# Kernel tuning notes

Hardware: AMD Instinct MI355X
Metric: run time of the kernel (lower is better)

The kernel has to match this reference:

```python
import jax, jax.numpy as jnp
import numpy as np

B, C, H, W = 16, 3, 224, 224
P = 16
DIM = 256
NL = 8
DS = 16          # d_state (mamba default)
DCONV = 4
NCLS = 1000
DI = 2 * DIM     # expand * dim
DTR = -(-DIM // 16)  # dt_rank = ceil(dim/16)
NPATCH = (H // P) * (W // P)
SEQ = NPATCH + 1


def _ln(x, g, b, eps=1e-5):
    mu = x.mean(-1, keepdims=True)
    var = ((x - mu) ** 2).mean(-1, keepdims=True)
    return (x - mu) * jax.lax.rsqrt(var + eps) * g + b


def setup_inputs() -> dict:
    key = jax.random.key(0)
    ks = jax.random.split(key, 12)
    pd = C * P * P
    s = 0.02
    return dict(
        img=jax.random.normal(ks[0], (B, C, H, W), jnp.float32),
        pe_ln1_g=jnp.ones((pd,), jnp.float32), pe_ln1_b=jnp.zeros((pd,), jnp.float32),
        pe_w=jax.random.normal(ks[1], (pd, DIM), jnp.float32) * s,
        pe_b=jnp.zeros((DIM,), jnp.float32),
        pe_ln2_g=jnp.ones((DIM,), jnp.float32), pe_ln2_b=jnp.zeros((DIM,), jnp.float32),
        pos_emb=jax.random.normal(ks[2], (1, SEQ, DIM), jnp.float32) * s,
        cls_tok=jax.random.normal(ks[3], (1, 1, DIM), jnp.float32) * s,
        ln_w=jnp.ones((NL, DIM), jnp.float32), ln_b=jnp.zeros((NL, DIM), jnp.float32),
        in_w=jax.random.normal(ks[4], (NL, DIM, 2 * DI), jnp.float32) * s,
        conv_w=jax.random.normal(ks[5], (NL, DI, DCONV), jnp.float32) * s,
        conv_b=jnp.zeros((NL, DI), jnp.float32),
        xproj_w=jax.random.normal(ks[6], (NL, DI, DTR + 2 * DS), jnp.float32) * s,
        dtproj_w=jax.random.normal(ks[7], (NL, DTR, DI), jnp.float32) * s,
        dtproj_b=jax.random.uniform(ks[8], (NL, DI), jnp.float32, -4.0, -2.0),
        A_log=jnp.log(jnp.broadcast_to(jnp.arange(1, DS + 1, dtype=jnp.float32), (NL, DI, DS))) + jnp.zeros((NL, DI, DS), jnp.float32),
        Dp=jnp.ones((NL, DI), jnp.float32),
        out_w=jax.random.normal(ks[9], (NL, DI, DIM), jnp.float32) * s,
        normf_w=jnp.ones((DIM,), jnp.float32), normf_b=jnp.zeros((DIM,), jnp.float32),
        head_w=jax.random.normal(ks[10], (DIM, NCLS), jnp.float32) * s,
        head_b=jnp.zeros((NCLS,), jnp.float32),
    )


def _mamba(x, in_w, conv_w, conv_b, xproj_w, dtproj_w, dtproj_b, A_log, Dp, out_w):
    b, L, _ = x.shape
    xz = x @ in_w                       # (b, L, 2*DI)
    xm, z = jnp.split(xz, 2, axis=-1)
    # causal depthwise conv1d (torch pads both sides then slices -> left-pad d_conv-1)
    xc = jnp.pad(xm.transpose(0, 2, 1), ((0, 0), (0, 0), (DCONV - 1, 0)))
    xc = jax.lax.conv_general_dilated(
        xc, conv_w[:, None, :], (1,), 'VALID',
        dimension_numbers=('NCH', 'OIH', 'NCH'), feature_group_count=DI)
    u = jax.nn.silu(xc + conv_b[None, :, None]).transpose(0, 2, 1)  # (b, L, DI)
    dbc = u @ xproj_w                   # (b, L, DTR+2*DS)
    dt, Bm, Cm = jnp.split(dbc, [DTR, DTR + DS], axis=-1)
    dt = jax.nn.softplus(dt @ dtproj_w + dtproj_b)  # (b, L, DI)
    A = -jnp.exp(A_log)                 # (DI, DS)

    def step(h, inp):
        dt_t, B_t, C_t, u_t = inp       # (b,DI), (b,DS), (b,DS), (b,DI)
        dA = jnp.exp(dt_t[:, :, None] * A)                 # (b, DI, DS)
        h = dA * h + (dt_t * u_t)[:, :, None] * B_t[:, None, :]
        y = jnp.einsum('bdn,bn->bd', h, C_t)
        return h, y

    h0 = jnp.zeros((b, DI, DS), x.dtype)
    xs = (dt.transpose(1, 0, 2), Bm.transpose(1, 0, 2),
          Cm.transpose(1, 0, 2), u.transpose(1, 0, 2))
    _, ys = jax.lax.scan(step, h0, xs)
    y = ys.transpose(1, 0, 2) + u * Dp  # (b, L, DI)
    y = y * jax.nn.silu(z)
    return y @ out_w                    # (b, L, DIM)


def reference(img, pe_ln1_g, pe_ln1_b, pe_w, pe_b, pe_ln2_g, pe_ln2_b, pos_emb,
              cls_tok, ln_w, ln_b, in_w, conv_w, conv_b, xproj_w, dtproj_w,
              dtproj_b, A_log, Dp, out_w, normf_w, normf_b, head_w, head_b):
    b = img.shape[0]
    h, w = H // P, W // P
    # 'b c (h p1) (w p2) -> b (h w) (p1 p2 c)'
    x = img.reshape(b, C, h, P, w, P).transpose(0, 2, 4, 3, 5, 1).reshape(b, h * w, P * P * C)
    x = _ln(x, pe_ln1_g, pe_ln1_b)
    x = x @ pe_w + pe_b
    x = _ln(x, pe_ln2_g, pe_ln2_b)
    x = jnp.concatenate([jnp.broadcast_to(cls_tok, (b, 1, DIM)), x], axis=1)
    x = x + pos_emb[:, :x.shape[1]]
    residual = None
    for i in range(NL):
        residual = x if residual is None else x + residual
        xn = _ln(residual, ln_w[i], ln_b[i])
        x = _mamba(xn, in_w[i], conv_w[i], conv_b[i], xproj_w[i],
                   dtproj_w[i], dtproj_b[i], A_log[i], Dp[i], out_w[i])
    residual = x + residual
    x = _ln(residual, normf_w, normf_b)
    x = x[:, 0]                          # pool == 'cls'
    return x @ head_w + head_b
```

## Files before the change

kernel.cpp:

```cpp
#include <hip/hip_runtime.h>
#include <math.h>

#define NB   16
#define SEQL 197
#define TB   (NB*SEQL)
#define DIMM 256
#define DI   512
#define DS   16
#define NL   8

typedef __bf16 bf16x8 __attribute__((ext_vector_type(8)));
typedef __bf16 bf16x4 __attribute__((ext_vector_type(4)));
typedef float floatx4 __attribute__((ext_vector_type(4)));

__device__ __forceinline__ void block_reduce_2(float& s1, float& s2, float* red, int tid){
  #pragma unroll
  for (int off = 32; off > 0; off >>= 1){
    s1 += __shfl_down(s1, off, 64);
    s2 += __shfl_down(s2, off, 64);
  }
  __syncthreads();
  if ((tid & 63) == 0){ red[(tid>>6)*2] = s1; red[(tid>>6)*2+1] = s2; }
  __syncthreads();
  s1 = red[0] + red[2] + red[4] + red[6];
  s2 = red[1] + red[3] + red[5] + red[7];
}

__global__ __launch_bounds__(256) void prep_weights(
    const float* __restrict__ in_w, const float* __restrict__ out_w,
    const float* __restrict__ pe_w, const float* __restrict__ xproj,
    __bf16* __restrict__ wt_in, __bf16* __restrict__ wt_out,
    __bf16* __restrict__ wt_pe, float* __restrict__ wt_xp_f)
{
  __shared__ float t[32][33];
  int bid = blockIdx.x;
  const float* src; __bf16* dst = nullptr; float* dstf = nullptr;
  int K, Nin, n0, k0;
  if (bid < 2048){
    int z = bid >> 8, tt = bid & 255;
    K = 256; Nin = 1024; n0 = (tt & 31)*32; k0 = (tt >> 5)*32;
    src = in_w  + (size_t)z*K*Nin;
    dst = wt_in + (size_t)z*K*Nin;
  } else if (bid < 3072){
    int t2 = bid - 2048; int z = t2 >> 7, tt = t2 & 127;
    K = 512; Nin = 256; n0 = (tt & 7)*32; k0 = (tt >> 3)*32;
    src = out_w  + (size_t)z*K*Nin;
    dst = wt_out + (size_t)z*K*Nin;
  } else if (bid < 3264){
    int tt = bid - 3072;
    K = 768; Nin = 256; n0 = (tt & 7)*32; k0 = (tt >> 3)*32;
    src = pe_w; dst = wt_pe;
  } else {
    int t2 = bid - 3264; int z = t2 >> 5, tt = t2 & 31;
    K = 512; Nin = 48; n0 = (tt & 1)*32; k0 = (tt >> 1)*32;
    src  = xproj + (size_t)z*K*Nin;
    dstf = wt_xp_f + (size_t)z*64*512;
  }
  int tx = threadIdx.x & 31, ty = threadIdx.x >> 5;
  #pragma unroll
  for (int j = 0; j < 4; j++){
    int n = n0 + tx;
    t[ty + j*8][tx] = (n < Nin) ? src[(size_t)(k0 + ty + j*8)*Nin + n] : 0.f;
  }
  __syncthreads();
  if (dstf){
    #pragma unroll
    for (int j = 0; j < 4; j++){
      int k = k0 + tx, c = n0 + ty + j*8;
      dstf[(size_t)(k>>2)*256 + c*4 + (k&3)] = t[tx][ty + j*8];
    }
  } else {
    #pragma unroll
    for (int j = 0; j < 4; j++)
      dst[(size_t)(n0 + ty + j*8)*K + k0 + tx] = (__bf16)t[tx][ty + j*8];
  }
}

template<int BM, int BN, int KS>
__global__ __launch_bounds__(256) void gemm_bf16(
    const __bf16* __restrict__ A, const __bf16* __restrict__ Wt,
    const float* __restrict__ bias, float* __restrict__ C, int M, int N, int K)
{
  constexpr int BK  = 32;
  constexpr int LDA = BK + 8;
  constexpr int TMW = BM/32;
  constexpr int TNW = BN/32;
  __shared__ __bf16 As[BM][LDA];
  __shared__ __bf16 Bs[BN][LDA];

  int tid  = threadIdx.x;
  int lane = tid & 63, w = tid >> 6;
  int wm = w >> 1, wn = w & 1;
  int l15 = lane & 15, quad = lane >> 4;
  int nt = blockIdx.x / KS, ks = blockIdx.x % KS;
  int bm = blockIdx.y * BM, bn = nt * BN;
  int kbeg = ks * (K / KS), kend = kbeg + (K / KS);

  floatx4 acc[TMW][TNW] = {};

  for (int k0 = kbeg; k0 < kend; k0 += BK){
    #pragma unroll
    for (int i = 0; i < BM/64; i++){
      int c = tid + i*256;
      int row = c >> 2, kc = c & 3;
      int m = bm + row;
      uint4 v = make_uint4(0,0,0,0);
      if (m < M) v = ((const uint4*)(A + (size_t)m*K + k0))[kc];
      *(uint4*)&As[row][kc*8] = v;
    }
    #pragma unroll
    for (int i = 0; i < BN/64; i++){
      int c = tid + i*256;
      int row = c >> 2, kc = c & 3;
      int n = bn + row;
      uint4 v = ((const uint4*)(Wt + (size_t)n*K + k0))[kc];
      *(uint4*)&Bs[row][kc*8] = v;
    }
    __syncthreads();
    bf16x8 af[TMW], bf[TNW];
    #pragma unroll
    for (int mi = 0; mi < TMW; mi++)
      af[mi] = *(const bf16x8*)&As[wm*(BM/2) + mi*16 + l15][quad*8];
    #pragma unroll
    for (int ni = 0; ni < TNW; ni++)
      bf[ni] = *(const bf16x8*)&Bs[wn*(BN/2) + ni*16 + l15][quad*8];
    #pragma unroll
    for (int mi = 0; mi < TMW; mi++)
      #pragma unroll
      for (int ni = 0; ni < TNW; ni++)
        acc[mi][ni] = __builtin_amdgcn_mfma_f32_16x16x32_bf16(af[mi], bf[ni], acc[mi][ni], 0, 0, 0);
    __syncthreads();
  }
  #pragma unroll
  for (int mi = 0; mi < TMW; mi++){
    #pragma unroll
    for (int ni = 0; ni < TNW; ni++){
      int col = bn + wn*(BN/2) + ni*16 + l15;
      float bv = (KS == 1 && bias) ? bias[col] : 0.f;
      #pragma unroll
      for (int r = 0; r < 4; r++){
        int row = bm + wm*(BM/2) + mi*16 + quad*4 + r;
        if (row < M){
          if (KS == 1) C[(size_t)row*N + col] = acc[mi][ni][r] + bv;
          else         atomicAdd(&C[(size_t)row*N + col], acc[mi][ni][r]);
        }
      }
    }
  }
}

template<int DO_LN>
__global__ __launch_bounds__(512) void gemm_out_fused(
    const __bf16* __restrict__ A, const __bf16* __restrict__ Wt,
    float* __restrict__ resid, __bf16* __restrict__ xn_bf,
    const float* __restrict__ g, const float* __restrict__ bta)
{
  constexpr int BK = 64, LDA = BK + 8;
  __shared__ alignas(16) char smem[(16 + 256) * LDA * sizeof(__bf16)];
  __bf16 (*As)[LDA] = (__bf16(*)[LDA])smem;
  __bf16 (*Bs)[LDA] = (__bf16(*)[LDA])(smem + 16*LDA*sizeof(__bf16));
  float  (*sy)[264] = (float(*)[264])smem;

  int tid = threadIdx.x, lane = tid & 63, w = tid >> 6;
  int l15 = lane & 15, quad = lane >> 4;
  int bm = blockIdx.x * 16;

  floatx4 acc[2] = {};
  for (int k0 = 0; k0 < 512; k0 += BK){
    if (tid < 128){
      int row = tid >> 3, kc = tid & 7;
      *(uint4*)&As[row][kc*8] = ((const uint4*)(A + (size_t)(bm+row)*512 + k0))[kc];
    }
    #pragma unroll
    for (int i = 0; i < 4; i++){
      int c = tid + i*512;
      int row = c >> 3, kc = c & 7;
      *(uint4*)&Bs[row][kc*8] = ((const uint4*)(Wt + (size_t)row*512 + k0))[kc];
    }
    __syncthreads();
    #pragma unroll
    for (int kk = 0; kk < 2; kk++){
      bf16x8 af = *(const bf16x8*)&As[l15][kk*32 + quad*8];
      #pragma unroll
      for (int ni = 0; ni < 2; ni++){
        bf16x8 bfv = *(const bf16x8*)&Bs[w*32 + ni*16 + l15][kk*32 + quad*8];
        acc[ni] = __builtin_amdgcn_mfma_f32_16x16x32_bf16(af, bfv, acc[ni], 0, 0, 0);
      }
    }
    __syncthreads();
  }
  #pragma unroll
  for (int ni = 0; ni < 2; ni++){
    int col = w*32 + ni*16 + l15;
    #pragma unroll
    for (int r = 0; r < 4; r++)
      sy[quad*4 + r][col] = acc[ni][r];
  }
  __syncthreads();
  #pragma unroll
  for (int rr = 0; rr < 2; rr++){
    int row = w*2 + rr;
    size_t base = (size_t)(bm + row)*256 + lane*4;
    float4 y4 = *(const float4*)&sy[row][lane*4];
    float4 rv = *(const float4*)&resid[base];
    float4 v;
    v.x = y4.x + rv.x; v.y = y4.y + rv.y; v.z = y4.z + rv.z; v.w = y4.w + rv.w;
    *(float4*)&resid[base] = v;
    if (DO_LN){
      float s  = v.x + v.y + v.z + v.w;
      float s2 = v.x*v.x + v.y*v.y + v.z*v.z + v.w*v.w;
      #pragma unroll
      for (int off = 1; off < 64; off <<= 1){
        s  += __shfl_xor(s,  off, 64);
        s2 += __shfl_xor(s2, off, 64);
      }
      float mu  = s * (1.f/256.f);
      float var = s2 * (1.f/256.f) - mu*mu;
      float rrq = rsqrtf(var + 1e-5f);
      float4 gv = *(const float4*)&g[lane*4];
      float4 bv = *(const float4*)&bta[lane*4];
      bf16x4 o;
      o[0] = (__bf16)((v.x - mu)*rrq*gv.x + bv.x);
      o[1] = (__bf16)((v.y - mu)*rrq*gv.y + bv.y);
      o[2] = (__bf16)((v.z - mu)*rrq*gv.z + bv.z);
      o[3] = (__bf16)((v.w - mu)*rrq*gv.w + bv.w);
      *(bf16x4*)&xn_bf[base] = o;
    }
  }
}

__global__ __launch_bounds__(256) void patch_ln1(
    const float* __restrict__ img, const float* __restrict__ g1, const float* __restrict__ b1,
    __bf16* __restrict__ xp_bf)
{
  __shared__ float red[8];
  int blk = blockIdx.x;
  int b = blk / 196, p = blk % 196;
  int hh = p / 14, ww = p % 14;
  int tid = threadIdx.x;

  float v[3]; float s = 0.f, s2 = 0.f;
  #pragma unroll
  for (int i = 0; i < 3; i++){
    int e  = tid + i*256;
    int c  = e % 3;
    int p2 = (e/3) % 16;
    int p1 = e / 48;
    float val = img[((b*3 + c)*224 + hh*16 + p1)*224 + ww*16 + p2];
    v[i] = val; s += val; s2 += val*val;
  }
  block_reduce_2(s, s2, red, tid);
  float mu = s * (1.f/768.f);
  float var = s2 * (1.f/768.f) - mu*mu;
  float rr = rsqrtf(var + 1e-5f);
  #pragma unroll
  for (int i = 0; i < 3; i++){
    int e = tid + i*256;
    xp_bf[(size_t)blk*768 + e] = (__bf16)((v[i] - mu) * rr * g1[e] + b1[e]);
  }
}

__global__ __launch_bounds__(256) void ln2_cls_pos(
    const float* __restrict__ pemb, const float* __restrict__ g2, const float* __restrict__ b2,
    const float* __restrict__ pos, const float* __restrict__ cls,
    float* __restrict__ resid,
    const float* __restrict__ g0, const float* __restrict__ b0,
    __bf16* __restrict__ xn_bf)
{
  __shared__ float red[8];
  int blk = blockIdx.x;
  int b = blk / SEQL, l = blk % SEQL;
  int tid = threadIdx.x;
  float o;
  if (l == 0){
    o = cls[tid] + pos[tid];
  } else {
    int p = l - 1;
    float v = pemb[(size_t)(b*196 + p)*256 + tid];
    float s = v, s2 = v*v;
    block_reduce_2(s, s2, red, tid);
    float mu = s * (1.f/256.f);
    float var = s2 * (1.f/256.f) - mu*mu;
    float rr = rsqrtf(var + 1e-5f);
    o = (v - mu) * rr * g2[tid] + b2[tid] + pos[l*256 + tid];
  }
  size_t idx = (size_t)blk*256 + tid;
  resid[idx] = o;
  float s = o, s2 = o*o;
  block_reduce_2(s, s2, red, tid);
  float mu = s * (1.f/256.f);
  float var = s2 * (1.f/256.f) - mu*mu;
  float rr = rsqrtf(var + 1e-5f);
  xn_bf[idx] = (__bf16)((o - mu) * rr * g0[tid] + b0[tid]);
}

__global__ __launch_bounds__(256) void conv_xproj(
    const float* __restrict__ xz, const float* __restrict__ cw, const float* __restrict__ cb,
    const float* __restrict__ wxp,
    float* __restrict__ u, float* __restrict__ dbc)
{
  __shared__ float s_u[8][512];
  __shared__ float s_acc[4][8][64];
  int tid = threadIdx.x;
  int t0 = blockIdx.x * 8;

  int d = (tid & 127) * 4;
  float4 w0 = *(const float4*)&cw[(d+0)*4];
  float4 w1 = *(const float4*)&cw[(d+1)*4];
  float4 w2 = *(const float4*)&cw[(d+2)*4];
  float4 w3 = *(const float4*)&cw[(d+3)*4];
  float4 cbv = *(const float4*)&cb[d];
  const float4 z4 = make_float4(0.f,0.f,0.f,0.f);
  int tt0 = t0 + (tid >> 7)*4;
  float4 h1 = (tt0 >= 1) ? *(const float4*)&xz[(size_t)(tt0-1)*1024 + d] : z4;
  float4 h2 = (tt0 >= 2) ? *(const float4*)&xz[(size_t)(tt0-2)*1024 + d] : z4;
  float4 h3 = (tt0 >= 3) ? *(const float4*)&xz[(size_t)(tt0-3)*1024 + d] : z4;
  int l0 = tt0 % SEQL;
  #pragma unroll
  for (int j = 0; j < 4; j++){
    int t = tt0 + j;
    int l = l0 + j; if (l >= SEQL) l -= SEQL;
    float4 x0 = *(const float4*)&xz[(size_t)t*1024 + d];
    float4 x1 = (l>=1) ? h1 : z4;
    float4 x2 = (l>=2) ? h2 : z4;
    float4 x3 = (l>=3) ? h3 : z4;
    float4 r = cbv;
    r.x += x3.x*w0.x + x2.x*w0.y + x1.x*w0.z + x0.x*w0.w;
    r.y += x3.y*w1.x + x2.y*w1.y + x1.y*w1.z + x0.y*w1.w;
    r.z += x3.z*w2.x + x2.z*w2.y + x1.z*w2.z + x0.z*w2.w;
    r.w += x3.w*w3.x + x2.w*w3.y + x1.w*w3.z + x0.w*w3.w;
    r.x *= 1.f/(1.f + __expf(-r.x));
    r.y *= 1.f/(1.f + __expf(-r.y));
    r.z *= 1.f/(1.f + __expf(-r.z));
    r.w *= 1.f/(1.f + __expf(-r.w));
    *(float4*)&u[(size_t)t*512 + d] = r;
    *(float4*)&s_u[(tid>>7)*4 + j][d] = r;
    h3 = h2; h2 = h1; h1 = x0;
  }
  __syncthreads();

  int col = tid & 63, sl = tid >> 6;
  const float4* wp4 = (const float4*)wxp + (size_t)sl*32*64 + col;
  float a[8] = {};
  #pragma unroll 4
  for (int k4 = 0; k4 < 32; k4++){
    float4 wv = wp4[(size_t)k4*64];
    #pragma unroll
    for (int t = 0; t < 8; t++){
      float4 v = *(const float4*)&s_u[t][sl*128 + k4*4];
      a[t] += wv.x*v.x + wv.y*v.y + wv.z*v.z + wv.w*v.w;
    }
  }
  #pragma unroll
  for (int t = 0; t < 8; t++) s_acc[sl][t][col] = a[t];
  __syncthreads();
  #pragma unroll
  for (int j = 0; j < 2; j++){
    int p = tid + j*256;
    int tok = p >> 6, c2 = p & 63;
    if (c2 < 48){
      float v = s_acc[0][tok][c2] + s_acc[1][tok][c2]
              + s_acc[2][tok][c2] + s_acc[3][tok][c2];
      dbc[(size_t)(t0 + tok)*64 + c2] = v;
    }
  }
}

#define SCT 32
#define NCH ((SEQL + SCT - 1)/SCT)
#define NDL 8
__global__ __launch_bounds__(128) void scan_kernel(
    const float* __restrict__ u, const float* __restrict__ dbc,
    const float* __restrict__ xz, const float* __restrict__ A_log, const float* __restrict__ Dp,
    const float* __restrict__ dtw, const float* __restrict__ dtb,
    __bf16* __restrict__ yg_bf)
{
  __shared__ float s_D [16][36];
  __shared__ float s_B [16][36];
  __shared__ float s_C [16][36];
  __shared__ float s_u [NDL][36];
  __shared__ float s_z [NDL][36];
  __shared__ float s_dt[NDL][36];
  __shared__ float s_yp[SCT][NDL][20];
  __shared__ float s_dp[NDL];

  int tid = threadIdx.x;
  int n = tid & 15, dl = tid >> 4;
  int b = blockIdx.x >> 6, dg = blockIdx.x & 63;
  int d0 = dg * NDL;
  const size_t base = (size_t)b * SEQL;

  float A = -__expf(A_log[(d0+dl)*DS + n]);
  float h = 0.f;
  if (tid < NDL) s_dp[tid] = Dp[d0 + tid];
  int cch = tid & 7;
  float wc[16];
  #pragma unroll
  for (int k = 0; k < 16; k++) wc[k] = dtw[k*512 + d0 + cch];
  float dtbv = dtb[d0 + cch];

  float r_u[2], r_z[2], r_db[12];
  auto load_regs = [&](int c){
    #pragma unroll
    for (int i = 0; i < 2; i++){
      int v = tid + i*128;
      int tg = c*SCT + (v>>3); if (tg > SEQL-1) tg = SEQL-1;
      size_t t = base + tg;
      r_u[i] = u [t*512 + d0 + (v&7)];
      r_z[i] = xz[t*1024 + 512 + d0 + (v&7)];
    }
    #pragma unroll
    for (int s = 0; s < 3; s++)
      #pragma unroll
      for (int i = 0; i < 4; i++){
        int v = tid + i*128;
        int tg = c*SCT + (v>>4); if (tg > SEQL-1) tg = SEQL-1;
        r_db[s*4+i] = dbc[(base + tg)*64 + s*16 + (v&15)];
      }
  };
  auto write_DBC = [&](){
    #pragma unroll
    for (int i = 0; i < 4; i++){
      int v = tid + i*128;
      s_D[v&15][v>>4] = r_db[0+i];
      s_B[v&15][v>>4] = r_db[4+i];
      s_C[v&15][v>>4] = r_db[8+i];
    }
  };
  auto write_UZ = [&](){
    #pragma unroll
    for (int i = 0; i < 2; i++){
      int v = tid + i*128;
      s_u[v&7][v>>3] = r_u[i];
      s_z[v&7][v>>3] = r_z[i];
    }
  };
  auto compute_dt = [&](){
    #pragma unroll
    for (int i = 0; i < 2; i++){
      int tl = (tid >> 3) + i*16;
      float acc = dtbv;
      #pragma unroll
      for (int k = 0; k < 16; k++) acc += s_D[k][tl] * wc[k];
      s_dt[cch][tl] = (acc > 20.f) ? acc : log1pf(__expf(acc));
    }
  };

  load_regs(0);
  write_DBC();
  write_UZ();
  __syncthreads();
  compute_dt();
  __syncthreads();

  for (int c = 0; c < NCH; c++){
    if (c + 1 < NCH) load_regs(c+1);

    float4 dt4, u4, B4, C4;
    #pragma unroll
    for (int tl = 0; tl < SCT; tl++){
      if ((tl & 3) == 0){
        dt4 = *(const float4*)&s_dt[dl][tl];
        u4  = *(const float4*)&s_u [dl][tl];
        B4  = *(const float4*)&s_B [n][tl];
        C4  = *(const float4*)&s_C [n][tl];
      }
      float dtv = ((float*)&dt4)[tl&3];
      float uv  = ((float*)&u4 )[tl&3];
      float Bv  = ((float*)&B4 )[tl&3];
      float Cv  = ((float*)&C4 )[tl&3];
      h = __expf(dtv * A) * h + (dtv * uv) * Bv;
      s_yp[tl][dl][n] = h * Cv;
    }
    __syncthreads();

    if (c + 1 < NCH) write_DBC();

    #pragma unroll
    for (int j = 0; j < 2; j++){
      int p = tid + j*128;
      int tl = p >> 3, dr = p & 7;
      float4 a0 = *(const float4*)&s_yp[tl][dr][0];
      float4 a1 = *(const float4*)&s_yp[tl][dr][4];
      float4 a2 = *(const float4*)&s_yp[tl][dr][8];
      float4 a3 = *(const float4*)&s_yp[tl][dr][12];
      float yv = ((a0.x+a0.y)+(a0.z+a0.w)) + ((a1.x+a1.y)+(a1.z+a1.w))
               + ((a2.x+a2.y)+(a2.z+a2.w)) + ((a3.x+a3.y)+(a3.z+a3.w));
      int tg = c*SCT + tl;
      if (tg < SEQL){
        float uv = s_u[dr][tl];
        float zv = s_z[dr][tl];
        float sg = 1.f / (1.f + __expf(-zv));
        yg_bf[(base + tg)*512 + d0 + dr] = (__bf16)((yv + uv*s_dp[dr]) * zv * sg);
      }
    }
    __syncthreads();

    if (c + 1 < NCH){
      write_UZ();
      compute_dt();
      __syncthreads();
    }
  }
}

__global__ __launch_bounds__(256) void final_head(
    const float* __restrict__ resid,
    const float* __restrict__ g, const float* __restrict__ bta,
    const float* __restrict__ head_w, const float* __restrict__ head_b,
    float* __restrict__ out)
{
  __shared__ float xs[16][256];
  int tid = threadIdx.x, lane = tid & 63, w = tid >> 6;
  #pragma unroll
  for (int rb = 0; rb < 4; rb++){
    int b = w + rb*4;
    const float* rp = resid + (size_t)b*SEQL*256;
    float4 v = *(const float4*)&rp[lane*4];
    float s  = v.x + v.y + v.z + v.w;
    float s2 = v.x*v.x + v.y*v.y + v.z*v.z + v.w*v.w;
    #pragma unroll
    for (int off = 1; off < 64; off <<= 1){
      s  += __shfl_xor(s,  off, 64);
      s2 += __shfl_xor(s2, off, 64);
    }
    float mu  = s * (1.f/256.f);
    float var = s2 * (1.f/256.f) - mu*mu;
    float rr  = rsqrtf(var + 1e-5f);
    float4 gv = *(const float4*)&g[lane*4];
    float4 bv = *(const float4*)&bta[lane*4];
    xs[b][lane*4+0] = (v.x - mu)*rr*gv.x + bv.x;
    xs[b][lane*4+1] = (v.y - mu)*rr*gv.y + bv.y;
    xs[b][lane*4+2] = (v.z - mu)*rr*gv.z + bv.z;
    xs[b][lane*4+3] = (v.w - mu)*rr*gv.w + bv.w;
  }
  __syncthreads();
  int nl = tid & 31, bq = tid >> 5;
  int nn = blockIdx.x*32 + nl;
  if (nn >= 1000) return;
  float acc0 = 0.f, acc1 = 0.f;
  #pragma unroll 8
  for (int k = 0; k < 256; k++){
    float wv = head_w[k*1000 + nn];
    acc0 += xs[bq][k]   * wv;
    acc1 += xs[bq+8][k] * wv;
  }
  float hb = head_b[nn];
  out[(size_t)bq*1000 + nn]     = acc0 + hb;
  out[(size_t)(bq+8)*1000 + nn] = acc1 + hb;
}

extern "C" void kernel_launch(void* const* d_in, const int* in_sizes, int n_in,
                              void* d_out, int out_size, void* d_ws, size_t ws_size,
                              hipStream_t stream) {
  const float* img   = (const float*)d_in[0];
  const float* ln1g  = (const float*)d_in[1];
  const float* ln1b  = (const float*)d_in[2];
  const float* pe_w  = (const float*)d_in[3];
  const float* pe_b  = (const float*)d_in[4];
  const float* ln2g  = (const float*)d_in[5];
  const float* ln2b  = (const float*)d_in[6];
  const float* pos   = (const float*)d_in[7];
  const float* cls   = (const float*)d_in[8];
  const float* ln_w  = (const float*)d_in[9];
  const float* ln_b  = (const float*)d_in[10];
  const float* in_w  = (const float*)d_in[11];
  const float* conv_w= (const float*)d_in[12];
  const float* conv_b= (const float*)d_in[13];
  const float* xproj = (const float*)d_in[14];
  const float* dtw   = (const float*)d_in[15];
  const float* dtb   = (const float*)d_in[16];
  const float* A_log = (const float*)d_in[17];
  const float* Dp    = (const float*)d_in[18];
  const float* out_w = (const float*)d_in[19];
  const float* nfw   = (const float*)d_in[20];
  const float* nfb   = (const float*)d_in[21];
  const float* head_w= (const float*)d_in[22];
  const float* head_b= (const float*)d_in[23];
  float* out = (float*)d_out;

  float* ws = (float*)d_ws;
  float* resid = ws;  ws += (size_t)TB*DIMM;
  float* xz    = ws;  ws += (size_t)TB*2*DI;
  float* u     = ws;  ws += (size_t)TB*DI;
  float* dbc   = ws;  ws += (size_t)TB*64;
  float* wt_xp_f = ws; ws += (size_t)NL*64*512;
  __bf16* xn_bf = (__bf16*)ws;  ws += (size_t)TB*DIMM/2;
  __bf16* yg_bf = (__bf16*)ws;  ws += (size_t)TB*DI/2;
  __bf16* wt_in = (__bf16*)ws;  ws += (size_t)NL*1024*256/2;
  __bf16* wt_out= (__bf16*)ws;  ws += (size_t)NL*256*512/2;
  __bf16* wt_pe = (__bf16*)ws;  ws += (size_t)256*768/2;
  __bf16* xp_bf = (__bf16*)xz;
  float*  pemb  = u;

  prep_weights<<<3520, 256, 0, stream>>>(in_w, out_w, pe_w, xproj,
                                          wt_in, wt_out, wt_pe, wt_xp_f);

  patch_ln1<<<NB*196, 256, 0, stream>>>(img, ln1g, ln1b, xp_bf);
  gemm_bf16<64,64,1><<<dim3(256/64, 3136/64), 256, 0, stream>>>(
      xp_bf, wt_pe, pe_b, pemb, 3136, 256, 768);
  ln2_cls_pos<<<NB*SEQL, 256, 0, stream>>>(pemb, ln2g, ln2b, pos, cls,
                                           resid, ln_w, ln_b, xn_bf);

  for (int i = 0; i < NL; i++){
    gemm_bf16<64,128,1><<<dim3(1024/128, (TB+63)/64), 256, 0, stream>>>(
        xn_bf, wt_in + (size_t)i*1024*256, nullptr, xz, TB, 1024, 256);
    conv_xproj<<<TB/8, 256, 0, stream>>>(
        xz, conv_w + i*DI*4, conv_b + i*DI, wt_xp_f + (size_t)i*64*512, u, dbc);
    scan_kernel<<<NB*64, 128, 0, stream>>>(
        u, dbc, xz, A_log + i*DI*DS, Dp + i*DI, dtw + i*16*DI, dtb + i*DI, yg_bf);
    if (i < NL-1)
      gemm_out_fused<1><<<TB/16, 512, 0, stream>>>(
          yg_bf, wt_out + (size_t)i*256*512, resid, xn_bf,
          ln_w + (i+1)*DIMM, ln_b + (i+1)*DIMM);
    else
      gemm_out_fused<0><<<TB/16, 512, 0, stream>>>(
          yg_bf, wt_out + (size_t)i*256*512, resid, nullptr, nullptr, nullptr);
  }
  final_head<<<(1000+31)/32, 256, 0, stream>>>(resid, nfw, nfb, head_w, head_b, out);
}
```

Before: 640.7 us.

## Prefetch GEMM tiles through registers, coalesce patch LN, use one wave per row

The bf16 GEMM now loads the next K-tile from global memory into registers while MFMAs run on the current LDS tile. The K-tile grows to 64 with an inner 32-step loop, and the unused split-K atomic path is removed. patch_ln1 now reads each pixel's three channels from contiguous rows, so image loads coalesce, and writes the permuted index directly. ln2_cls_pos handles one token per wave with float4 loads and shuffle reductions instead of block-wide reductions. The register prefetch raises register pressure, and the GEMMs plus LN kernels are a small share of the total time next to the scan.

After: 683.4 us. 1.07x slower.

```diff
diff --git a/kernel.cpp b/kernel.cpp
--- a/kernel.cpp
+++ b/kernel.cpp
@@ -76,15 +76,17 @@
   }
 }
 
-template<int BM, int BN, int KS>
+template<int BM, int BN, int BK>
 __global__ __launch_bounds__(256) void gemm_bf16(
     const __bf16* __restrict__ A, const __bf16* __restrict__ Wt,
     const float* __restrict__ bias, float* __restrict__ C, int M, int N, int K)
 {
-  constexpr int BK  = 32;
   constexpr int LDA = BK + 8;
   constexpr int TMW = BM/32;
   constexpr int TNW = BN/32;
+  constexpr int KU  = BK/8;
+  constexpr int NA  = BM*KU/256;
+  constexpr int NBu = BN*KU/256;
   __shared__ __bf16 As[BM][LDA];
   __shared__ __bf16 Bs[BN][LDA];
 
@@ -92,43 +94,60 @@
   int lane = tid & 63, w = tid >> 6;
   int wm = w >> 1, wn = w & 1;
   int l15 = lane & 15, quad = lane >> 4;
-  int nt = blockIdx.x / KS, ks = blockIdx.x % KS;
-  int bm = blockIdx.y * BM, bn = nt * BN;
-  int kbeg = ks * (K / KS), kend = kbeg + (K / KS);
+  int bm = blockIdx.y * BM, bn = blockIdx.x * BN;
 
   floatx4 acc[TMW][TNW] = {};
-
-  for (int k0 = kbeg; k0 < kend; k0 += BK){
-    #pragma unroll
-    for (int i = 0; i < BM/64; i++){
+  uint4 pa[NA], pb[NBu];
+
+  auto load_regs = [&](int k0){
+    #pragma unroll
+    for (int i = 0; i < NA; i++){
       int c = tid + i*256;
-      int row = c >> 2, kc = c & 3;
+      int row = c / KU, kc = c % KU;
       int m = bm + row;
-      uint4 v = make_uint4(0,0,0,0);
-      if (m < M) v = ((const uint4*)(A + (size_t)m*K + k0))[kc];
-      *(uint4*)&As[row][kc*8] = v;
-    }
-    #pragma unroll
-    for (int i = 0; i < BN/64; i++){
+      pa[i] = make_uint4(0,0,0,0);
+      if (m < M) pa[i] = ((const uint4*)(A + (size_t)m*K + k0))[kc];
+    }
+    #pragma unroll
+    for (int i = 0; i < NBu; i++){
       int c = tid + i*256;
-      int row = c >> 2, kc = c & 3;
-      int n = bn + row;
-      uint4 v = ((const uint4*)(Wt + (size_t)n*K + k0))[kc];
-      *(uint4*)&Bs[row][kc*8] = v;
-    }
+      int row = c / KU, kc = c % KU;
+      pb[i] = ((const uint4*)(Wt + (size_t)(bn + row)*K + k0))[kc];
+    }
+  };
+  auto store_lds = [&](){
+    #pragma unroll
+    for (int i = 0; i < NA; i++){
+      int c = tid + i*256;
+      *(uint4*)&As[c / KU][(c % KU)*8] = pa[i];
+    }
+    #pragma unroll
+    for (int i = 0; i < NBu; i++){
+      int c = tid + i*256;
+      *(uint4*)&Bs[c / KU][(c % KU)*8] = pb[i];
+    }
+  };
+
+  load_regs(0);
+  for (int k0 = 0; k0 < K; k0 += BK){
+    store_lds();
     __syncthreads();
-    bf16x8 af[TMW], bf[TNW];
-    #pragma unroll
-    for (int mi = 0; mi < TMW; mi++)
-      af[mi] = *(const bf16x8*)&As[wm*(BM/2) + mi*16 + l15][quad*8];
-    #pragma unroll
-    for (int ni = 0; ni < TNW; ni++)
-      bf[ni] = *(const bf16x8*)&Bs[wn*(BN/2) + ni*16 + l15][quad*8];
-    #pragma unroll
-    for (int mi = 0; mi < TMW; mi++)
+    if (k0 + BK < K) load_regs(k0 + BK);
+    #pragma unroll
+    for (int kk = 0; kk < BK/32; kk++){
+      bf16x8 af[TMW], bf[TNW];
+      #pragma unroll
+      for (int mi = 0; mi < TMW; mi++)
+        af[mi] = *(const bf16x8*)&As[wm*(BM/2) + mi*16 + l15][kk*32 + quad*8];
       #pragma unroll
       for (int ni = 0; ni < TNW; ni++)
-        acc[mi][ni] = __builtin_amdgcn_mfma_f32_16x16x32_bf16(af[mi], bf[ni], acc[mi][ni], 0, 0, 0);
+        bf[ni] = *(const bf16x8*)&Bs[wn*(BN/2) + ni*16 + l15][kk*32 + quad*8];
+      #pragma unroll
+      for (int mi = 0; mi < TMW; mi++)
+        #pragma unroll
+        for (int ni = 0; ni < TNW; ni++)
+          acc[mi][ni] = __builtin_amdgcn_mfma_f32_16x16x32_bf16(af[mi], bf[ni], acc[mi][ni], 0, 0, 0);
+    }
     __syncthreads();
   }
   #pragma unroll
@@ -136,14 +155,11 @@
     #pragma unroll
     for (int ni = 0; ni < TNW; ni++){
       int col = bn + wn*(BN/2) + ni*16 + l15;
-      float bv = (KS == 1 && bias) ? bias[col] : 0.f;
+      float bv = bias ? bias[col] : 0.f;
       #pragma unroll
       for (int r = 0; r < 4; r++){
         int row = bm + wm*(BM/2) + mi*16 + quad*4 + r;
-        if (row < M){
-          if (KS == 1) C[(size_t)row*N + col] = acc[mi][ni][r] + bv;
-          else         atomicAdd(&C[(size_t)row*N + col], acc[mi][ni][r]);
-        }
+        if (row < M) C[(size_t)row*N + col] = acc[mi][ni][r] + bv;
       }
     }
   }
@@ -239,24 +255,21 @@
   int hh = p / 14, ww = p % 14;
   int tid = threadIdx.x;
 
+  const float* ip = img + ((size_t)(b*3)*224 + hh*16 + (tid>>4))*224 + ww*16 + (tid&15);
   float v[3]; float s = 0.f, s2 = 0.f;
   #pragma unroll
-  for (int i = 0; i < 3; i++){
-    int e  = tid + i*256;
-    int c  = e % 3;
-    int p2 = (e/3) % 16;
-    int p1 = e / 48;
-    float val = img[((b*3 + c)*224 + hh*16 + p1)*224 + ww*16 + p2];
-    v[i] = val; s += val; s2 += val*val;
+  for (int c = 0; c < 3; c++){
+    float val = ip[(size_t)c*224*224];
+    v[c] = val; s += val; s2 += val*val;
   }
   block_reduce_2(s, s2, red, tid);
   float mu = s * (1.f/768.f);
   float var = s2 * (1.f/768.f) - mu*mu;
   float rr = rsqrtf(var + 1e-5f);
   #pragma unroll
-  for (int i = 0; i < 3; i++){
-    int e = tid + i*256;
-    xp_bf[(size_t)blk*768 + e] = (__bf16)((v[i] - mu) * rr * g1[e] + b1[e]);
+  for (int c = 0; c < 3; c++){
+    int e = tid*3 + c;
+    xp_bf[(size_t)blk*768 + e] = (__bf16)((v[c] - mu) * rr * g1[e] + b1[e]);
   }
 }
 
@@ -267,31 +280,55 @@
     const float* __restrict__ g0, const float* __restrict__ b0,
     __bf16* __restrict__ xn_bf)
 {
-  __shared__ float red[8];
-  int blk = blockIdx.x;
+  int w = threadIdx.x >> 6, lane = threadIdx.x & 63;
+  int blk = blockIdx.x*4 + w;
   int b = blk / SEQL, l = blk % SEQL;
-  int tid = threadIdx.x;
-  float o;
+  int e = lane*4;
+  float4 o;
   if (l == 0){
-    o = cls[tid] + pos[tid];
+    float4 cv = *(const float4*)&cls[e];
+    float4 pv = *(const float4*)&pos[e];
+    o.x = cv.x + pv.x; o.y = cv.y + pv.y; o.z = cv.z + pv.z; o.w = cv.w + pv.w;
   } else {
-    int p = l - 1;
-    float v = pemb[(size_t)(b*196 + p)*256 + tid];
-    float s = v, s2 = v*v;
-    block_reduce_2(s, s2, red, tid);
-    float mu = s * (1.f/256.f);
+    float4 v = *(const float4*)&pemb[(size_t)(b*196 + l-1)*256 + e];
+    float s  = v.x + v.y + v.z + v.w;
+    float s2 = v.x*v.x + v.y*v.y + v.z*v.z + v.w*v.w;
+    #pragma unroll
+    for (int off = 1; off < 64; off <<= 1){
+      s  += __shfl_xor(s,  off, 64);
+      s2 += __shfl_xor(s2, off, 64);
+    }
+    float mu  = s * (1.f/256.f);
     float var = s2 * (1.f/256.f) - mu*mu;
-    float rr = rsqrtf(var + 1e-5f);
-    o = (v - mu) * rr * g2[tid] + b2[tid] + pos[l*256 + tid];
-  }
-  size_t idx = (size_t)blk*256 + tid;
-  resid[idx] = o;
-  float s = o, s2 = o*o;
-  block_reduce_2(s, s2, red, tid);
-  float mu = s * (1.f/256.f);
+    float rr  = rsqrtf(var + 1e-5f);
+    float4 gv = *(const float4*)&g2[e];
+    float4 bv = *(const float4*)&b2[e];
+    float4 pv = *(const float4*)&pos[l*256 + e];
+    o.x = (v.x - mu)*rr*gv.x + bv.x + pv.x;
+    o.y = (v.y - mu)*rr*gv.y + bv.y + pv.y;
+    o.z = (v.z - mu)*rr*gv.z + bv.z + pv.z;
+    o.w = (v.w - mu)*rr*gv.w + bv.w + pv.w;
+  }
+  size_t idx = (size_t)blk*256 + e;
+  *(float4*)&resid[idx] = o;
+  float s  = o.x + o.y + o.z + o.w;
+  float s2 = o.x*o.x + o.y*o.y + o.z*o.z + o.w*o.w;
+  #pragma unroll
+  for (int off = 1; off < 64; off <<= 1){
+    s  += __shfl_xor(s,  off, 64);
+    s2 += __shfl_xor(s2, off, 64);
+  }
+  float mu  = s * (1.f/256.f);
   float var = s2 * (1.f/256.f) - mu*mu;
-  float rr = rsqrtf(var + 1e-5f);
-  xn_bf[idx] = (__bf16)((o - mu) * rr * g0[tid] + b0[tid]);
+  float rr  = rsqrtf(var + 1e-5f);
+  float4 gv = *(const float4*)&g0[e];
+  float4 bv = *(const float4*)&b0[e];
+  bf16x4 ob;
+  ob[0] = (__bf16)((o.x - mu)*rr*gv.x + bv.x);
+  ob[1] = (__bf16)((o.y - mu)*rr*gv.y + bv.y);
+  ob[2] = (__bf16)((o.z - mu)*rr*gv.z + bv.z);
+  ob[3] = (__bf16)((o.w - mu)*rr*gv.w + bv.w);
+  *(bf16x4*)&xn_bf[idx] = ob;
 }
 
 __global__ __launch_bounds__(256) void conv_xproj(
@@ -597,13 +634,13 @@
                                           wt_in, wt_out, wt_pe, wt_xp_f);
 
   patch_ln1<<<NB*196, 256, 0, stream>>>(img, ln1g, ln1b, xp_bf);
-  gemm_bf16<64,64,1><<<dim3(256/64, 3136/64), 256, 0, stream>>>(
+  gemm_bf16<64,64,64><<<dim3(4, 49), 256, 0, stream>>>(
       xp_bf, wt_pe, pe_b, pemb, 3136, 256, 768);
-  ln2_cls_pos<<<NB*SEQL, 256, 0, stream>>>(pemb, ln2g, ln2b, pos, cls,
-                                           resid, ln_w, ln_b, xn_bf);
+  ln2_cls_pos<<<TB/4, 256, 0, stream>>>(pemb, ln2g, ln2b, pos, cls,
+                                        resid, ln_w, ln_b, xn_bf);
 
   for (int i = 0; i < NL; i++){
-    gemm_bf16<64,128,1><<<dim3(1024/128, (TB+63)/64), 256, 0, stream>>>(
+    gemm_bf16<64,128,64><<<dim3(8, 50), 256, 0, stream>>>(
         xn_bf, wt_in + (size_t)i*1024*256, nullptr, xz, TB, 1024, 256);
     conv_xproj<<<TB/8, 256, 0, stream>>>(
         xz, conv_w + i*DI*4, conv_b + i*DI, wt_xp_f + (size_t)i*64*512, u, dbc);
```
